# Kernel tuning notes

Measured on AMD Instinct MI355X. Metric: run time of the kernel, lower is better.

The kernel has to match this reference:

```python
import jax, jax.numpy as jnp
import numpy as np

B, N, F, F1 = 1024, 75, 512, 256
NEG = -1.0e9
ALPHA = 0.2  # LeakyReLU slope


def setup_inputs() -> dict:
    key = jax.random.key(0)
    k1, k2, k3, k4 = jax.random.split(key, 4)
    X = jax.random.normal(k1, (B, N, F), dtype=jnp.float32)
    A = jax.random.randint(k2, (N, N), 0, 2, dtype=jnp.int32)  # binary adjacency
    W = jax.random.normal(k3, (F, F1), dtype=jnp.float32) * (1.0 / np.sqrt(F))
    a = jax.random.normal(k4, (2, F1, 1), dtype=jnp.float32) * (1.0 / np.sqrt(F1))
    return {"X": X, "A": A, "W": W, "a": a}


def reference(X, A, W, a):
    # Linear projection: [B, N, F1]
    h = jnp.einsum('bnf,fo->bno', X, W)
    # Additive attention logits
    att_self = jnp.einsum('bno,od->bnd', h, a[0])        # [B, N, 1]
    att_neigh = jnp.einsum('bno,od->bnd', h, a[1])       # [B, N, 1]
    e = att_self + jnp.swapaxes(att_neigh, 1, 2)         # [B, N, N]
    e = jax.nn.leaky_relu(e, ALPHA)
    # Adjacency mask: disallowed edges get large negative bias
    adj = A.astype(h.dtype)                               # [N, N]
    e = e + NEG * (1.0 - adj)[None, :, :]
    # Normalize over neighbors, aggregate
    alpha = jax.nn.softmax(e, axis=-1)                    # [B, N, N]
    out = jnp.einsum('bij,bjo->bio', alpha, h)            # [B, N, F1]
    return jnp.concatenate([out, h], axis=-1)             # [B, N, 2*F1]
```

## Files before the change

### kernel.cpp

```cpp
#include <hip/hip_runtime.h>
#include <hip/hip_bf16.h>
#include <math.h>

typedef __bf16 bf16_t;
typedef __bf16 bf16x4_t __attribute__((ext_vector_type(4)));
typedef __bf16 bf16x8 __attribute__((ext_vector_type(8)));
typedef float f32x4 __attribute__((ext_vector_type(4)));
typedef unsigned long long u64;

#define NB 1024
#define NN 75
#define KF 512
#define F1 256
#define HSTR 100
#define ASTR 100

__global__ __launch_bounds__(256) void wt_kernel(const float* __restrict__ W,
                                                 bf16_t* __restrict__ Wt) {
    __shared__ float tile[64][65];
    const int kb = blockIdx.x * 64;
    const int nb = blockIdx.y * 64;
    const int tc = threadIdx.x & 63;
    const int tr = threadIdx.x >> 6;
#pragma unroll
    for (int r = tr; r < 64; r += 4)
        tile[r][tc] = W[(size_t)(kb + r) * F1 + nb + tc];
    __syncthreads();
#pragma unroll
    for (int r = tr; r < 64; r += 4)
        Wt[(size_t)(nb + r) * KF + kb + tc] = (bf16_t)tile[tc][r];
}

__global__ __launch_bounds__(256) void gemm_kernel(const float* __restrict__ X,
                                                   const bf16_t* __restrict__ Wt,
                                                   float* __restrict__ out) {
    __shared__ __align__(16) bf16_t Xs[64 * 512];

    const int t = threadIdx.x;
    const int w = t >> 6;
    const int l = t & 63;
    const int lc = l & 15;
    const int lr = l >> 4;
    const int m0 = blockIdx.x * 64;

    const bf16_t* wp0 = Wt + (size_t)(w * 64 +  0 + lc) * KF + lr * 8;
    const bf16_t* wp1 = Wt + (size_t)(w * 64 + 16 + lc) * KF + lr * 8;
    const bf16_t* wp2 = Wt + (size_t)(w * 64 + 32 + lc) * KF + lr * 8;
    const bf16_t* wp3 = Wt + (size_t)(w * 64 + 48 + lc) * KF + lr * 8;

    bf16x8 wA[4], wB[4];
#define WLOAD(WREG, KS)                                        \
    WREG[0] = *(const bf16x8*)(wp0 + (KS) * 32);               \
    WREG[1] = *(const bf16x8*)(wp1 + (KS) * 32);               \
    WREG[2] = *(const bf16x8*)(wp2 + (KS) * 32);               \
    WREG[3] = *(const bf16x8*)(wp3 + (KS) * 32);

    WLOAD(wA, 0);

    const float* Xbase = X + (size_t)m0 * KF;
#pragma unroll
    for (int q = 0; q < 16; ++q) {
        const int r = q * 4 + w;
        const float* rp = Xbase + (size_t)r * KF + l * 8;
        const float4 a = *(const float4*)rp;
        const float4 b = *(const float4*)(rp + 4);
        bf16x8 v;
        v[0] = (bf16_t)a.x; v[1] = (bf16_t)a.y;
        v[2] = (bf16_t)a.z; v[3] = (bf16_t)a.w;
        v[4] = (bf16_t)b.x; v[5] = (bf16_t)b.y;
        v[6] = (bf16_t)b.z; v[7] = (bf16_t)b.w;
        *(bf16x8*)&Xs[r * 512 + ((l ^ (r & 7)) * 8)] = v;
    }
    __syncthreads();

    f32x4 acc[4][4];
#pragma unroll
    for (int i = 0; i < 4; ++i)
#pragma unroll
        for (int j = 0; j < 4; ++j) acc[i][j] = (f32x4){0.f, 0.f, 0.f, 0.f};

#define GSTEP(KS, WREG)                                                        \
    {                                                                          \
        bf16x8 af[4];                                                          \
        _Pragma("unroll")                                                      \
        for (int mt = 0; mt < 4; ++mt) {                                       \
            const int row = mt * 16 + lc;                                      \
            const int ch = ((KS) * 4 + lr) ^ (lc & 7);                         \
            af[mt] = *(const bf16x8*)&Xs[row * 512 + ch * 8];                  \
        }                                                                      \
        _Pragma("unroll")                                                      \
        for (int mt = 0; mt < 4; ++mt)                                         \
            _Pragma("unroll")                                                  \
            for (int ntl = 0; ntl < 4; ++ntl)                                  \
                acc[mt][ntl] = __builtin_amdgcn_mfma_f32_16x16x32_bf16(        \
                    af[mt], WREG[ntl], acc[mt][ntl], 0, 0, 0);                 \
    }

#pragma unroll
    for (int kp = 0; kp < 8; ++kp) {
        const int ks0 = kp * 2;
        const int ks1 = kp * 2 + 1;
        WLOAD(wB, ks1);
        GSTEP(ks0, wA);
        if (ks1 < 15) { WLOAD(wA, ks1 + 1); }
        GSTEP(ks1, wB);
    }
#undef GSTEP
#undef WLOAD

#pragma unroll
    for (int mt = 0; mt < 4; ++mt) {
#pragma unroll
        for (int ntl = 0; ntl < 4; ++ntl) {
            const int col = w * 64 + ntl * 16 + lc;
#pragma unroll
            for (int j = 0; j < 4; ++j) {
                const int row = m0 + mt * 16 + lr * 4 + j;
                out[(size_t)row * 512 + 256 + col] = acc[mt][ntl][j];
            }
        }
    }
}

__global__ __launch_bounds__(256) void pv_kernel(const int* __restrict__ Adj,
                                                 const float* __restrict__ avec,
                                                 float* __restrict__ out) {
    __shared__ __align__(16) bf16_t hT[256 * HSTR];
    __shared__ __align__(16) bf16_t alp[80 * ASTR];
    __shared__ float a0s[F1], a1s[F1];
    __shared__ float attp0[4][80], attp1[4][80];
    __shared__ float att0s[80], att1s[80], rsums[80];
    __shared__ u64 adjb[160];

    const int b = blockIdx.x;
    const int t = threadIdx.x;
    const int w = t >> 6;
    const int l = t & 63;
    const int lc = l & 15;
    const int lr = l >> 4;
    float* outb = out + (size_t)b * NN * 512;

    a0s[t] = avec[t];
    a1s[t] = avec[F1 + t];
    for (int i = w; i < NN; i += 4) {
        const int v0 = Adj[i * NN + l];
        const int v1 = (l < NN - 64) ? Adj[i * NN + 64 + l] : 0;
        const u64 b0 = __ballot(v0 != 0);
        const u64 b1 = __ballot(v1 != 0);
        if (l == 0) { adjb[i * 2] = b0; adjb[i * 2 + 1] = b1; }
    }
    {
        int* z = (int*)&hT[t * HSTR + 80];
#pragma unroll
        for (int k = 0; k < 8; ++k) z[k] = 0;
    }
    __syncthreads();

    const int c0 = w * 64 + lc * 4;
    const float4 a04 = *(const float4*)&a0s[c0];
    const float4 a14 = *(const float4*)&a1s[c0];
#pragma unroll
    for (int jp = 0; jp < 5; ++jp) {
        const int j0 = jp * 16 + lr * 4;
        float hr[4][4];
#pragma unroll
        for (int r = 0; r < 4; ++r) {
            if (j0 + r < NN) {
                const float4 v = *(const float4*)(outb + (size_t)(j0 + r) * 512 + 256 + c0);
                hr[r][0] = v.x; hr[r][1] = v.y; hr[r][2] = v.z; hr[r][3] = v.w;
            } else {
                hr[r][0] = hr[r][1] = hr[r][2] = hr[r][3] = 0.f;
            }
        }
        float p0[4], p1[4];
#pragma unroll
        for (int r = 0; r < 4; ++r) {
            p0[r] = hr[r][0] * a04.x + hr[r][1] * a04.y + hr[r][2] * a04.z + hr[r][3] * a04.w;
            p1[r] = hr[r][0] * a14.x + hr[r][1] * a14.y + hr[r][2] * a14.z + hr[r][3] * a14.w;
        }
#pragma unroll
        for (int off = 1; off < 16; off <<= 1) {
#pragma unroll
            for (int r = 0; r < 4; ++r) {
                p0[r] += __shfl_xor(p0[r], off);
                p1[r] += __shfl_xor(p1[r], off);
            }
        }
        if (lc == 0) {
#pragma unroll
            for (int r = 0; r < 4; ++r) {
                attp0[w][j0 + r] = p0[r];
                attp1[w][j0 + r] = p1[r];
            }
        }
#pragma unroll
        for (int cc = 0; cc < 4; ++cc) {
            bf16x4_t v;
            v[0] = (bf16_t)hr[0][cc]; v[1] = (bf16_t)hr[1][cc];
            v[2] = (bf16_t)hr[2][cc]; v[3] = (bf16_t)hr[3][cc];
            *(bf16x4_t*)&hT[(c0 + cc) * HSTR + j0] = v;
        }
    }
    __syncthreads();

    if (t < 80)
        att0s[t] = attp0[0][t] + attp0[1][t] + attp0[2][t] + attp0[3][t];
    else if (t < 160)
        att1s[t - 80] = attp1[0][t - 80] + attp1[1][t - 80] + attp1[2][t - 80] + attp1[3][t - 80];
    else if (t < 240) {
        const int r = t - 160;
        if (r < NN) {
            for (int c = NN; c < 96; ++c) alp[r * ASTR + c] = (bf16_t)0.f;
        } else {
            for (int c = 0; c < 96; ++c) alp[r * ASTR + c] = (bf16_t)0.f;
        }
    }
    __syncthreads();

    {
        const int gid = t >> 2;
        const int k4 = t & 3;
#pragma unroll
        for (int r = 0; r < 2; ++r) {
            const int i = r * 64 + gid;
            if (i < NN) {
                const float a0i = att0s[i];
                const u64 w0 = adjb[i * 2];
                const u64 w1 = adjb[i * 2 + 1];
                float e[19];
                float m = -3.0e38f;
#pragma unroll
                for (int jj = 0; jj < 19; ++jj) {
                    const int j = jj * 4 + k4;
                    float ev = -3.0e38f;
                    if (j < NN) {
                        float x = a0i + att1s[j];
                        x = x > 0.f ? x : 0.2f * x;
                        const u64 wj = (j < 64) ? w0 : w1;
                        const int bit = (int)((wj >> (j & 63)) & 1);
                        ev = bit ? x : x - 1.0e9f;
                    }
                    e[jj] = ev;
                    m = fmaxf(m, ev);
                }
                m = fmaxf(m, __shfl_xor(m, 1));
                m = fmaxf(m, __shfl_xor(m, 2));
                float s = 0.f;
#pragma unroll
                for (int jj = 0; jj < 19; ++jj) {
                    const int j = jj * 4 + k4;
                    if (j < NN) {
                        const float ex = __expf(e[jj] - m);
                        s += ex;
                        alp[i * ASTR + j] = (bf16_t)ex;
                    }
                }
                s += __shfl_xor(s, 1);
                s += __shfl_xor(s, 2);
                if (k4 == 0) rsums[i] = 1.f / s;
            }
        }
    }
    __syncthreads();

    f32x4 acc2[5][4];
#pragma unroll
    for (int i = 0; i < 5; ++i)
#pragma unroll
        for (int j = 0; j < 4; ++j) acc2[i][j] = (f32x4){0.f, 0.f, 0.f, 0.f};

#pragma unroll
    for (int ks = 0; ks < 3; ++ks) {
        bf16x8 bv[4];
#pragma unroll
        for (int ntl = 0; ntl < 4; ++ntl) {
            const bf16_t* q = &hT[(w * 64 + ntl * 16 + lc) * HSTR + ks * 32 + lr * 8];
            ((uint2*)&bv[ntl])[0] = *(const uint2*)q;
            ((uint2*)&bv[ntl])[1] = *(const uint2*)(q + 4);
        }
#pragma unroll
        for (int mt = 0; mt < 5; ++mt) {
            const bf16_t* ap = &alp[(mt * 16 + lc) * ASTR + ks * 32 + lr * 8];
            bf16x8 av;
            ((uint2*)&av)[0] = *(const uint2*)ap;
            ((uint2*)&av)[1] = *(const uint2*)(ap + 4);
#pragma unroll
            for (int ntl = 0; ntl < 4; ++ntl)
                acc2[mt][ntl] = __builtin_amdgcn_mfma_f32_16x16x32_bf16(av, bv[ntl], acc2[mt][ntl], 0, 0, 0);
        }
    }

#pragma unroll
    for (int mt = 0; mt < 5; ++mt) {
#pragma unroll
        for (int j = 0; j < 4; ++j) {
            const int row = mt * 16 + lr * 4 + j;
            if (row < NN) {
                const float rsv = rsums[row];
#pragma unroll
                for (int ntl = 0; ntl < 4; ++ntl) {
                    const int ch = w * 64 + ntl * 16 + lc;
                    outb[(size_t)row * 512 + ch] = acc2[mt][ntl][j] * rsv;
                }
            }
        }
    }
}

extern "C" void kernel_launch(void* const* d_in, const int* in_sizes, int n_in,
                              void* d_out, int out_size, void* d_ws, size_t ws_size,
                              hipStream_t stream) {
    const float* X = (const float*)d_in[0];
    const int*   A = (const int*)d_in[1];
    const float* W = (const float*)d_in[2];
    const float* a = (const float*)d_in[3];
    float* out = (float*)d_out;
    bf16_t* Wt = (bf16_t*)d_ws;

    wt_kernel<<<dim3(KF / 64, F1 / 64), 256, 0, stream>>>(W, Wt);
    gemm_kernel<<<(NB * NN) / 64, 256, 0, stream>>>(X, Wt, out);
    pv_kernel<<<NB, 256, 0, stream>>>(A, a, out);
}
```

Baseline: 131.6 us.

## Make projection GEMM persistent with double-buffered async global-to-LDS X loads

The projection GEMM now runs as a persistent grid of 512 blocks that loop over the 1200 row tiles. It streams X in K-chunks of 128 fp32 directly into LDS with global_load_lds, using a two-buffer pipeline that prefetches the next chunk or the next tile while MFMAs run. Conversion to bf16 moves from the staging step to the LDS read step. The intent is to overlap X loads with compute and remove the per-block load-then-compute stall. The cost is an fp32 LDS layout that doubles LDS read traffic, extra conversion work in the inner loop, and a barrier per chunk.

```diff
diff --git a/kernel.cpp b/kernel.cpp
--- a/kernel.cpp
+++ b/kernel.cpp
@@ -7,6 +7,9 @@
 typedef __bf16 bf16x8 __attribute__((ext_vector_type(8)));
 typedef float f32x4 __attribute__((ext_vector_type(4)));
 typedef unsigned long long u64;
+
+typedef __attribute__((address_space(1))) const unsigned int cu32_g;
+typedef __attribute__((address_space(3))) unsigned int u32_s;
 
 #define NB 1024
 #define NN 75
@@ -14,6 +17,8 @@
 #define F1 256
 #define HSTR 100
 #define ASTR 100
+#define NT 1200
+#define GRID 512
 
 __global__ __launch_bounds__(256) void wt_kernel(const float* __restrict__ W,
                                                  bf16_t* __restrict__ Wt) {
@@ -31,23 +36,21 @@
         Wt[(size_t)(nb + r) * KF + kb + tc] = (bf16_t)tile[tc][r];
 }
 
-__global__ __launch_bounds__(256) void gemm_kernel(const float* __restrict__ X,
-                                                   const bf16_t* __restrict__ Wt,
-                                                   float* __restrict__ out) {
-    __shared__ __align__(16) bf16_t Xs[64 * 512];
+__global__ __launch_bounds__(256, 2) void gemm_kernel(const float* __restrict__ X,
+                                                      const bf16_t* __restrict__ Wt,
+                                                      float* __restrict__ out) {
+    __shared__ __align__(16) float Xs[2][64 * 128];
 
     const int t = threadIdx.x;
     const int w = t >> 6;
     const int l = t & 63;
     const int lc = l & 15;
     const int lr = l >> 4;
-    const int m0 = blockIdx.x * 64;
 
     const bf16_t* wp0 = Wt + (size_t)(w * 64 +  0 + lc) * KF + lr * 8;
     const bf16_t* wp1 = Wt + (size_t)(w * 64 + 16 + lc) * KF + lr * 8;
     const bf16_t* wp2 = Wt + (size_t)(w * 64 + 32 + lc) * KF + lr * 8;
     const bf16_t* wp3 = Wt + (size_t)(w * 64 + 48 + lc) * KF + lr * 8;
-
     bf16x8 wA[4], wB[4];
 #define WLOAD(WREG, KS)                                        \
     WREG[0] = *(const bf16x8*)(wp0 + (KS) * 32);               \
@@ -55,38 +58,36 @@
     WREG[2] = *(const bf16x8*)(wp2 + (KS) * 32);               \
     WREG[3] = *(const bf16x8*)(wp3 + (KS) * 32);
 
-    WLOAD(wA, 0);
-
-    const float* Xbase = X + (size_t)m0 * KF;
-#pragma unroll
-    for (int q = 0; q < 16; ++q) {
-        const int r = q * 4 + w;
-        const float* rp = Xbase + (size_t)r * KF + l * 8;
-        const float4 a = *(const float4*)rp;
-        const float4 b = *(const float4*)(rp + 4);
-        bf16x8 v;
-        v[0] = (bf16_t)a.x; v[1] = (bf16_t)a.y;
-        v[2] = (bf16_t)a.z; v[3] = (bf16_t)a.w;
-        v[4] = (bf16_t)b.x; v[5] = (bf16_t)b.y;
-        v[6] = (bf16_t)b.z; v[7] = (bf16_t)b.w;
-        *(bf16x8*)&Xs[r * 512 + ((l ^ (r & 7)) * 8)] = v;
-    }
-    __syncthreads();
+    const int sl31 = l & 31;
+#define ISSUE(BUF, TILE, C)                                                    \
+    {                                                                          \
+        _Pragma("unroll")                                                      \
+        for (int u = 0; u < 8; ++u) {                                          \
+            const int rowl = u * 8 + w * 2 + (l >> 5);                         \
+            const float* g = X + ((size_t)(TILE) * 64 + rowl) * KF             \
+                              + (C) * 128 + ((sl31 ^ (rowl & 7)) << 2);        \
+            float* lp = &Xs[BUF][(u * 8 + w * 2) * 128];                       \
+            __builtin_amdgcn_global_load_lds((cu32_g*)g, (u32_s*)lp, 16, 0, 0);\
+        }                                                                      \
+    }
 
     f32x4 acc[4][4];
-#pragma unroll
-    for (int i = 0; i < 4; ++i)
-#pragma unroll
-        for (int j = 0; j < 4; ++j) acc[i][j] = (f32x4){0.f, 0.f, 0.f, 0.f};
-
-#define GSTEP(KS, WREG)                                                        \
+
+#define GSTEP(BUF, KS, WREG)                                                   \
     {                                                                          \
         bf16x8 af[4];                                                          \
         _Pragma("unroll")                                                      \
         for (int mt = 0; mt < 4; ++mt) {                                       \
             const int row = mt * 16 + lc;                                      \
-            const int ch = ((KS) * 4 + lr) ^ (lc & 7);                         \
-            af[mt] = *(const bf16x8*)&Xs[row * 512 + ch * 8];                  \
+            const int s0 = ((KS) & 3) * 8 + lr * 2;                            \
+            const f32x4 fa = *(const f32x4*)&Xs[BUF][row * 128 +               \
+                                                 ((s0 ^ (lc & 7)) << 2)];      \
+            const f32x4 fb = *(const f32x4*)&Xs[BUF][row * 128 +               \
+                                                 (((s0 + 1) ^ (lc & 7)) << 2)];\
+            af[mt][0] = (bf16_t)fa[0]; af[mt][1] = (bf16_t)fa[1];              \
+            af[mt][2] = (bf16_t)fa[2]; af[mt][3] = (bf16_t)fa[3];              \
+            af[mt][4] = (bf16_t)fb[0]; af[mt][5] = (bf16_t)fb[1];              \
+            af[mt][6] = (bf16_t)fb[2]; af[mt][7] = (bf16_t)fb[3];              \
         }                                                                      \
         _Pragma("unroll")                                                      \
         for (int mt = 0; mt < 4; ++mt)                                         \
@@ -96,30 +97,66 @@
                     af[mt], WREG[ntl], acc[mt][ntl], 0, 0, 0);                 \
     }
 
-#pragma unroll
-    for (int kp = 0; kp < 8; ++kp) {
-        const int ks0 = kp * 2;
-        const int ks1 = kp * 2 + 1;
-        WLOAD(wB, ks1);
-        GSTEP(ks0, wA);
-        if (ks1 < 15) { WLOAD(wA, ks1 + 1); }
-        GSTEP(ks1, wB);
-    }
+#define FENCE_SWAP()                                                           \
+    asm volatile("s_waitcnt vmcnt(0)" ::: "memory");                           \
+    __builtin_amdgcn_s_barrier();                                              \
+    __builtin_amdgcn_sched_barrier(0);
+
+#define CHUNK(C, TILE)                                                         \
+    {                                                                          \
+        if ((C) < 3) {                                                         \
+            ISSUE(((C) + 1) & 1, TILE, (C) + 1);                               \
+        } else if ((TILE) + GRID < NT) {                                       \
+            ISSUE(0, (TILE) + GRID, 0);                                        \
+        }                                                                      \
+        __builtin_amdgcn_sched_barrier(0);                                     \
+        WLOAD(wB, (C) * 4 + 1);                                                \
+        GSTEP((C) & 1, (C) * 4 + 0, wA);                                       \
+        WLOAD(wA, (C) * 4 + 2);                                                \
+        GSTEP((C) & 1, (C) * 4 + 1, wB);                                       \
+        WLOAD(wB, (C) * 4 + 3);                                                \
+        GSTEP((C) & 1, (C) * 4 + 2, wA);                                       \
+        WLOAD(wA, ((C) * 4 + 4) & 15);                                         \
+        GSTEP((C) & 1, (C) * 4 + 3, wB);                                       \
+        FENCE_SWAP();                                                          \
+    }
+
+    WLOAD(wA, 0);
+    int tile = blockIdx.x;
+    ISSUE(0, tile, 0);
+    FENCE_SWAP();
+
+    while (tile < NT) {
+#pragma unroll
+        for (int i = 0; i < 4; ++i)
+#pragma unroll
+            for (int j = 0; j < 4; ++j) acc[i][j] = (f32x4){0.f, 0.f, 0.f, 0.f};
+
+        CHUNK(0, tile);
+        CHUNK(1, tile);
+        CHUNK(2, tile);
+        CHUNK(3, tile);
+
+        const int m0 = tile * 64;
+#pragma unroll
+        for (int mt = 0; mt < 4; ++mt) {
+#pragma unroll
+            for (int ntl = 0; ntl < 4; ++ntl) {
+                const int col = w * 64 + ntl * 16 + lc;
+#pragma unroll
+                for (int j = 0; j < 4; ++j) {
+                    const int row = m0 + mt * 16 + lr * 4 + j;
+                    out[(size_t)row * 512 + 256 + col] = acc[mt][ntl][j];
+                }
+            }
+        }
+        tile += GRID;
+    }
+#undef CHUNK
+#undef FENCE_SWAP
 #undef GSTEP
+#undef ISSUE
 #undef WLOAD
-
-#pragma unroll
-    for (int mt = 0; mt < 4; ++mt) {
-#pragma unroll
-        for (int ntl = 0; ntl < 4; ++ntl) {
-            const int col = w * 64 + ntl * 16 + lc;
-#pragma unroll
-            for (int j = 0; j < 4; ++j) {
-                const int row = m0 + mt * 16 + lr * 4 + j;
-                out[(size_t)row * 512 + 256 + col] = acc[mt][ntl][j];
-            }
-        }
-    }
 }
 
 __global__ __launch_bounds__(256) void pv_kernel(const int* __restrict__ Adj,
@@ -318,6 +355,6 @@
     bf16_t* Wt = (bf16_t*)d_ws;
 
     wt_kernel<<<dim3(KF / 64, F1 / 64), 256, 0, stream>>>(W, Wt);
-    gemm_kernel<<<(NB * NN) / 64, 256, 0, stream>>>(X, Wt, out);
+    gemm_kernel<<<GRID, 256, 0, stream>>>(X, Wt, out);
     pv_kernel<<<NB, 256, 0, stream>>>(A, a, out);
 }
```

Result: faster. 125.1 us, median of 2 (-4.9%).

## Warp-specialize GEMM with producer waves streaming X into LDS ring

Applied to the files above, without the earlier changes.

The projection GEMM now runs 512 threads per block. Four producer waves stream fp32 X tiles into a four-slot LDS ring using direct global-to-LDS loads, and four consumer waves convert to bf16 and run MFMA. Hand-off uses ready/done flags with workgroup-scope atomics, replacing the single upfront load-convert-sync phase. The aim is to overlap X loading with compute and drop the register round trip. The cost is spin-wait overhead and a deadlock risk if the flag protocol is wrong.

```diff
diff --git a/kernel.cpp b/kernel.cpp
--- a/kernel.cpp
+++ b/kernel.cpp
@@ -7,6 +7,9 @@
 typedef __bf16 bf16x8 __attribute__((ext_vector_type(8)));
 typedef float f32x4 __attribute__((ext_vector_type(4)));
 typedef unsigned long long u64;
+
+typedef __attribute__((address_space(1))) const unsigned int cu32_g;
+typedef __attribute__((address_space(3))) unsigned int u32_s;
 
 #define NB 1024
 #define NN 75
@@ -31,92 +34,121 @@
         Wt[(size_t)(nb + r) * KF + kb + tc] = (bf16_t)tile[tc][r];
 }
 
-__global__ __launch_bounds__(256) void gemm_kernel(const float* __restrict__ X,
-                                                   const bf16_t* __restrict__ Wt,
-                                                   float* __restrict__ out) {
-    __shared__ __align__(16) bf16_t Xs[64 * 512];
+__global__ __launch_bounds__(512, 4) void gemm_kernel(const float* __restrict__ X,
+                                                      const bf16_t* __restrict__ Wt,
+                                                      float* __restrict__ out) {
+    __shared__ __align__(16) float Xs[4][64 * 64];
+    __shared__ int ready[4][4];
+    __shared__ int done[4][4];
 
     const int t = threadIdx.x;
     const int w = t >> 6;
     const int l = t & 63;
     const int lc = l & 15;
     const int lr = l >> 4;
-    const int m0 = blockIdx.x * 64;
-
-    const bf16_t* wp0 = Wt + (size_t)(w * 64 +  0 + lc) * KF + lr * 8;
-    const bf16_t* wp1 = Wt + (size_t)(w * 64 + 16 + lc) * KF + lr * 8;
-    const bf16_t* wp2 = Wt + (size_t)(w * 64 + 32 + lc) * KF + lr * 8;
-    const bf16_t* wp3 = Wt + (size_t)(w * 64 + 48 + lc) * KF + lr * 8;
-
-    bf16x8 wA[4], wB[4];
+    const int tile = blockIdx.x;
+    const size_t rbase = (size_t)tile * 64;
+
+    if (t < 16) { ready[t >> 2][t & 3] = -1; done[t >> 2][t & 3] = -1; }
+    __syncthreads();
+
+    if (w >= 4) {
+        const int p = w - 4;
+        for (int s = 0; s < 8; ++s) {
+            const int slot = s & 3;
+            if (s >= 4) {
+#pragma unroll
+                for (int c = 0; c < 4; ++c)
+                    while (__hip_atomic_load(&done[slot][c], __ATOMIC_ACQUIRE,
+                                             __HIP_MEMORY_SCOPE_WORKGROUP) < s - 4) {}
+            }
+#pragma unroll
+            for (int u = 0; u < 4; ++u) {
+                const int row = p * 16 + u * 4 + (l >> 4);
+                const float* g = X + (rbase + row) * KF + s * 64
+                                 + (((l & 15) ^ (row & 7)) << 2);
+                float* lp = &Xs[slot][(p * 16 + u * 4) * 64];
+                __builtin_amdgcn_global_load_lds((cu32_g*)g, (u32_s*)lp, 16, 0, 0);
+            }
+            if (s > 0) {
+                asm volatile("s_waitcnt vmcnt(4)" ::: "memory");
+                __hip_atomic_store(&ready[(s - 1) & 3][p], s - 1,
+                                   __ATOMIC_RELEASE, __HIP_MEMORY_SCOPE_WORKGROUP);
+            }
+        }
+        asm volatile("s_waitcnt vmcnt(0)" ::: "memory");
+        __hip_atomic_store(&ready[3][p], 7, __ATOMIC_RELEASE,
+                           __HIP_MEMORY_SCOPE_WORKGROUP);
+    } else {
+        const bf16_t* wp0 = Wt + (size_t)(w * 64 +  0 + lc) * KF + lr * 8;
+        const bf16_t* wp1 = Wt + (size_t)(w * 64 + 16 + lc) * KF + lr * 8;
+        const bf16_t* wp2 = Wt + (size_t)(w * 64 + 32 + lc) * KF + lr * 8;
+        const bf16_t* wp3 = Wt + (size_t)(w * 64 + 48 + lc) * KF + lr * 8;
+        bf16x8 wA[4], wB[4];
 #define WLOAD(WREG, KS)                                        \
-    WREG[0] = *(const bf16x8*)(wp0 + (KS) * 32);               \
-    WREG[1] = *(const bf16x8*)(wp1 + (KS) * 32);               \
-    WREG[2] = *(const bf16x8*)(wp2 + (KS) * 32);               \
-    WREG[3] = *(const bf16x8*)(wp3 + (KS) * 32);
-
-    WLOAD(wA, 0);
-
-    const float* Xbase = X + (size_t)m0 * KF;
-#pragma unroll
-    for (int q = 0; q < 16; ++q) {
-        const int r = q * 4 + w;
-        const float* rp = Xbase + (size_t)r * KF + l * 8;
-        const float4 a = *(const float4*)rp;
-        const float4 b = *(const float4*)(rp + 4);
-        bf16x8 v;
-        v[0] = (bf16_t)a.x; v[1] = (bf16_t)a.y;
-        v[2] = (bf16_t)a.z; v[3] = (bf16_t)a.w;
-        v[4] = (bf16_t)b.x; v[5] = (bf16_t)b.y;
-        v[6] = (bf16_t)b.z; v[7] = (bf16_t)b.w;
-        *(bf16x8*)&Xs[r * 512 + ((l ^ (r & 7)) * 8)] = v;
-    }
-    __syncthreads();
-
-    f32x4 acc[4][4];
-#pragma unroll
-    for (int i = 0; i < 4; ++i)
-#pragma unroll
-        for (int j = 0; j < 4; ++j) acc[i][j] = (f32x4){0.f, 0.f, 0.f, 0.f};
-
-#define GSTEP(KS, WREG)                                                        \
-    {                                                                          \
-        bf16x8 af[4];                                                          \
-        _Pragma("unroll")                                                      \
-        for (int mt = 0; mt < 4; ++mt) {                                       \
-            const int row = mt * 16 + lc;                                      \
-            const int ch = ((KS) * 4 + lr) ^ (lc & 7);                         \
-            af[mt] = *(const bf16x8*)&Xs[row * 512 + ch * 8];                  \
-        }                                                                      \
-        _Pragma("unroll")                                                      \
-        for (int mt = 0; mt < 4; ++mt)                                         \
+        WREG[0] = *(const bf16x8*)(wp0 + (KS) * 32);           \
+        WREG[1] = *(const bf16x8*)(wp1 + (KS) * 32);           \
+        WREG[2] = *(const bf16x8*)(wp2 + (KS) * 32);           \
+        WREG[3] = *(const bf16x8*)(wp3 + (KS) * 32);
+
+        f32x4 acc[4][4];
+#pragma unroll
+        for (int i = 0; i < 4; ++i)
+#pragma unroll
+            for (int j = 0; j < 4; ++j) acc[i][j] = (f32x4){0.f, 0.f, 0.f, 0.f};
+
+#define GSTEP(SLOT, KS, WREG)                                                  \
+        {                                                                      \
+            bf16x8 af[4];                                                      \
             _Pragma("unroll")                                                  \
-            for (int ntl = 0; ntl < 4; ++ntl)                                  \
-                acc[mt][ntl] = __builtin_amdgcn_mfma_f32_16x16x32_bf16(        \
-                    af[mt], WREG[ntl], acc[mt][ntl], 0, 0, 0);                 \
-    }
-
-#pragma unroll
-    for (int kp = 0; kp < 8; ++kp) {
-        const int ks0 = kp * 2;
-        const int ks1 = kp * 2 + 1;
-        WLOAD(wB, ks1);
-        GSTEP(ks0, wA);
-        if (ks1 < 15) { WLOAD(wA, ks1 + 1); }
-        GSTEP(ks1, wB);
-    }
+            for (int mt = 0; mt < 4; ++mt) {                                   \
+                const int row = mt * 16 + lc;                                  \
+                const int g0 = (KS) * 8 + lr * 2;                              \
+                const f32x4 fa = *(const f32x4*)&Xs[SLOT][row * 64 +           \
+                                      ((g0 ^ (lc & 7)) << 2)];                 \
+                const f32x4 fb = *(const f32x4*)&Xs[SLOT][row * 64 +           \
+                                      (((g0 + 1) ^ (lc & 7)) << 2)];           \
+                af[mt][0] = (bf16_t)fa[0]; af[mt][1] = (bf16_t)fa[1];          \
+                af[mt][2] = (bf16_t)fa[2]; af[mt][3] = (bf16_t)fa[3];          \
+                af[mt][4] = (bf16_t)fb[0]; af[mt][5] = (bf16_t)fb[1];          \
+                af[mt][6] = (bf16_t)fb[2]; af[mt][7] = (bf16_t)fb[3];          \
+            }                                                                  \
+            _Pragma("unroll")                                                  \
+            for (int mt = 0; mt < 4; ++mt)                                     \
+                _Pragma("unroll")                                              \
+                for (int ntl = 0; ntl < 4; ++ntl)                              \
+                    acc[mt][ntl] = __builtin_amdgcn_mfma_f32_16x16x32_bf16(    \
+                        af[mt], WREG[ntl], acc[mt][ntl], 0, 0, 0);             \
+        }
+
+        WLOAD(wA, 0);
+#pragma unroll
+        for (int s = 0; s < 8; ++s) {
+            const int slot = s & 3;
+#pragma unroll
+            for (int p = 0; p < 4; ++p)
+                while (__hip_atomic_load(&ready[slot][p], __ATOMIC_ACQUIRE,
+                                         __HIP_MEMORY_SCOPE_WORKGROUP) < s) {}
+            WLOAD(wB, s * 2 + 1);
+            GSTEP(slot, 0, wA);
+            if (s < 7) { WLOAD(wA, s * 2 + 2); }
+            GSTEP(slot, 1, wB);
+            __hip_atomic_store(&done[slot][w], s, __ATOMIC_RELEASE,
+                               __HIP_MEMORY_SCOPE_WORKGROUP);
+        }
 #undef GSTEP
 #undef WLOAD
 
 #pragma unroll
-    for (int mt = 0; mt < 4; ++mt) {
-#pragma unroll
-        for (int ntl = 0; ntl < 4; ++ntl) {
-            const int col = w * 64 + ntl * 16 + lc;
-#pragma unroll
-            for (int j = 0; j < 4; ++j) {
-                const int row = m0 + mt * 16 + lr * 4 + j;
-                out[(size_t)row * 512 + 256 + col] = acc[mt][ntl][j];
+        for (int mt = 0; mt < 4; ++mt) {
+#pragma unroll
+            for (int ntl = 0; ntl < 4; ++ntl) {
+                const int col = w * 64 + ntl * 16 + lc;
+#pragma unroll
+                for (int j = 0; j < 4; ++j) {
+                    const size_t row = rbase + mt * 16 + lr * 4 + j;
+                    out[row * 512 + 256 + col] = acc[mt][ntl][j];
+                }
             }
         }
     }
@@ -318,6 +350,6 @@
     bf16_t* Wt = (bf16_t*)d_ws;
 
     wt_kernel<<<dim3(KF / 64, F1 / 64), 256, 0, stream>>>(W, Wt);
-    gemm_kernel<<<(NB * NN) / 64, 256, 0, stream>>>(X, Wt, out);
+    gemm_kernel<<<(NB * NN) / 64, 512, 0, stream>>>(X, Wt, out);
     pv_kernel<<<NB, 256, 0, stream>>>(A, a, out);
 }
```

New measurement: 138.0 us. 4.9% more time.
